# Kernel tuning notes

Hardware: AMD Instinct MI355X
Metric: run time of the kernel (lower is better)

## Reference

```python
import jax, jax.numpy as jnp
import numpy as np

NPOINT = 1024
BRANCHES = [(0.4, 32), (0.8, 64)]  # (radius, nsample)
SPECS = [[67, 64, 64, 128], [67, 64, 128, 256]]  # mlp specs after use_xyz (+3)
EPS = 1e-5


def setup_inputs() -> dict:
    key = jax.random.key(0)
    ks = jax.random.split(key, 16)
    B, N, C = 8, 8192, 64
    inp = {
        "xyz": jax.random.normal(ks[0], (B, N, 3), jnp.float32),
        "features": jax.random.normal(ks[1], (B, C, N), jnp.float32),
    }
    ki = 2
    for bi, spec in enumerate(SPECS):
        for li in range(3):
            o, i = spec[li + 1], spec[li]
            inp[f"w{bi}_{li}"] = jax.random.normal(ks[ki], (o, i), jnp.float32) * (1.0 / np.sqrt(i)); ki += 1
            inp[f"g{bi}_{li}"] = jnp.ones((o,), jnp.float32)
            inp[f"b{bi}_{li}"] = jnp.zeros((o,), jnp.float32)
    return inp


def fps(pts, npoint):
    # pts: [B, N+1, 3] (mean point prepended); sequential farthest point sampling
    B, N1, _ = pts.shape

    def step(carry, _):
        dist, far = carry
        idx3 = jnp.broadcast_to(far[:, None, None], (B, 1, 3))
        centroid = jnp.take_along_axis(pts, idx3, axis=1)  # [B,1,3]
        d = jnp.sum((pts - centroid) ** 2, axis=-1)        # [B,N+1]
        dist = jnp.minimum(dist, d)
        far2 = jnp.argmax(dist, axis=-1)
        return (dist, far2), centroid[:, 0, :]

    dist0 = jnp.full((B, N1), 1e10, jnp.float32)
    far0 = jnp.zeros((B,), jnp.int32)
    _, locs = jax.lax.scan(step, (dist0, far0), None, length=npoint)
    return jnp.transpose(locs, (1, 0, 2))  # [B, npoint, 3]


def ball_query(xyz, new_xyz, radius, nsample):
    # first <=nsample indices with dist^2 < radius^2, padded with first valid (0 if none)
    B, N, _ = xyz.shape
    d2 = jnp.sum((new_xyz[:, :, None, :] - xyz[:, None, :, :]) ** 2, axis=-1)  # [B,S,N]
    score = jnp.where(d2 < radius * radius, jnp.arange(N, dtype=jnp.int32), N)
    vals, _ = jax.lax.top_k(-score, nsample)  # smallest scores = earliest valid indices
    idx = -vals                               # [B,S,nsample], N marks invalid
    first = idx[..., :1]
    first = jnp.where(first < N, first, 0)
    return jnp.where(idx < N, idx, first)


def _forward(xyz, features, params):
    mean = jnp.mean(xyz, axis=1, keepdims=True)
    pts = jnp.concatenate([mean, xyz], axis=1)          # prepend mean point
    new_xyz = jax.lax.stop_gradient(fps(pts, NPOINT))   # [B,npoint,3] (torch no_grad)
    outs = []
    for (radius, nsample), layers in zip(BRANCHES, params):
        idx = ball_query(xyz, new_xyz, radius, nsample)           # [B,S,K]
        gxyz = jax.vmap(lambda p, i: p[i])(xyz, idx)              # [B,S,K,3]
        rel = jnp.transpose(gxyz - new_xyz[:, :, None, :], (0, 3, 1, 2))  # [B,3,S,K]
        gfeat = jax.vmap(lambda f, i: f[:, i])(features, idx)     # [B,C,S,K]
        x = jnp.concatenate([rel, gfeat], axis=1)                 # [B,3+C,S,K]
        for W, g, b in layers:  # Conv2d 1x1 (no bias) + BatchNorm (train stats) + ReLU
            x = jnp.einsum('oi,bisk->bosk', W, x)
            m = jnp.mean(x, axis=(0, 2, 3), keepdims=True)
            v = jnp.var(x, axis=(0, 2, 3), keepdims=True)
            x = (x - m) / jnp.sqrt(v + EPS) * g[None, :, None, None] + b[None, :, None, None]
            x = jax.nn.relu(x)
        outs.append(jnp.max(x, axis=3))                           # [B,Cout,S]
    return new_xyz, jnp.concatenate(outs, axis=1)


def reference(xyz, features,
              w0_0, g0_0, b0_0, w0_1, g0_1, b0_1, w0_2, g0_2, b0_2,
              w1_0, g1_0, b1_0, w1_1, g1_1, b1_1, w1_2, g1_2, b1_2):
    params = [
        [(w0_0, g0_0, b0_0), (w0_1, g0_1, b0_1), (w0_2, g0_2, b0_2)],
        [(w1_0, g1_0, b1_0), (w1_1, g1_1, b1_1), (w1_2, g1_2, b1_2)],
    ]
    return _forward(xyz, features, params)
```

## Files before the change

kernel.cpp:

```cpp
#include <hip/hip_runtime.h>
#include <hip/hip_bf16.h>
#include <cstdint>


typedef __attribute__((ext_vector_type(8))) short short8;
typedef __attribute__((ext_vector_type(4))) float f32x4;
typedef __attribute__((ext_vector_type(2))) float f32x2;

__device__ __forceinline__ float bf2f(unsigned short u) {
    return __uint_as_float(((unsigned)u) << 16);
}
__device__ __forceinline__ unsigned short f2bf(float f) {
    unsigned u = __float_as_uint(f);
    return (unsigned short)((u + 0x7fffu + ((u >> 16) & 1u)) >> 16);
}

__device__ __forceinline__ float wave_red_max_f32(float v) {
#define DPPSTEP(ctrl)                                                                  \
    {                                                                                  \
        int _t = __builtin_amdgcn_update_dpp((int)0xFF800000, __float_as_int(v), ctrl, \
                                             0xf, 0xf, false);                         \
        v = fmaxf(v, __int_as_float(_t));                                              \
    }
    DPPSTEP(0x111) DPPSTEP(0x112) DPPSTEP(0x114) DPPSTEP(0x118) DPPSTEP(0x142) DPPSTEP(0x143)
#undef DPPSTEP
    return v;
}
__device__ __forceinline__ unsigned wave_red_min_u32(unsigned v) {
#define DPPSTEP(ctrl)                                                                   \
    {                                                                                   \
        unsigned _t = (unsigned)__builtin_amdgcn_update_dpp((int)0xFFFFFFFF, (int)v,    \
                                                            ctrl, 0xf, 0xf, false);     \
        v = v < _t ? v : _t;                                                            \
    }
    DPPSTEP(0x111) DPPSTEP(0x112) DPPSTEP(0x114) DPPSTEP(0x118) DPPSTEP(0x142) DPPSTEP(0x143)
#undef DPPSTEP
    return v;
}
__device__ __forceinline__ unsigned long long u64max(unsigned long long a, unsigned long long b) {
    return a > b ? a : b;
}
__device__ __forceinline__ unsigned u32min(unsigned a, unsigned b) { return a < b ? a : b; }

static const size_t OFF_WBF   = 0;
static const size_t OFF_STATS = 262144;
static const size_t STATS_BYTES = 720896;
static const size_t OFF_AFF   = 1048576;
static const size_t OFF_IDX0  = 2097152;
static const size_t OFF_IDX1  = 3145728;
static const size_t OFF_MX    = 5242880;
static const size_t OFF_MN    = 13631488;
static const size_t OFF_Y0    = 22020096;
static const size_t OFF_Y1    = 90177536;
static const size_t OFF_FEATT = 211812352;

__global__ __launch_bounds__(512) void fused_pre(
    const float* __restrict__ xyz, const float* __restrict__ feat,
    float* __restrict__ newxyz, unsigned short* __restrict__ ft,
    const float* __restrict__ w0, const float* __restrict__ w1, const float* __restrict__ w2,
    const float* __restrict__ w3, const float* __restrict__ w4, const float* __restrict__ w5,
    unsigned short* __restrict__ wb) {
    __shared__ union alignas(16) SM {
        struct {
            float ptsx[8200], ptsy[8200], ptsz[8200];
            float ldsM[16][3];
            float meanv[3];
            unsigned long long sKey[2][8];
            float cbuf[3072];
        } f;
        float tile[64][65];
    } sm;
    const int tid = threadIdx.x;

    if (blockIdx.x >= 1032) {
        int id = (int)(blockIdx.x - 1032) * 512 + tid;
        const int psz[6] = {6144, 4096, 8192, 6144, 8192, 32768};
        const int Kp[6] = {96, 64, 64, 96, 64, 128};
        const int Ks[6] = {67, 64, 64, 67, 64, 128};
        const float* wp[6] = {w0, w1, w2, w3, w4, w5};
        int off = 0;
        for (int l = 0; l < 6; ++l) {
            if (id < off + psz[l]) {
                int e = id - off;
                int m = e / Kp[l], k = e - m * Kp[l];
                float v = (k < Ks[l]) ? wp[l][m * Ks[l] + k] : 0.f;
                wb[id] = f2bf(v);
                return;
            }
            off += psz[l];
        }
        return;
    }

    if (blockIdx.x >= 8) {
        int tb = (int)blockIdx.x - 8;
        int b = tb >> 7;
        int j0 = (tb & 127) * 64;
#pragma unroll
        for (int i = 0; i < 8; ++i) {
            int e = i * 512 + tid;
            int c = e >> 6, j = e & 63;
            sm.tile[j][c] = feat[((size_t)b * 64 + c) * 8192 + j0 + j];
        }
        __syncthreads();
#pragma unroll
        for (int i = 0; i < 8; ++i) {
            int e = i * 512 + tid;
            int j = e >> 6, c = e & 63;
            ft[((size_t)(b * 8192 + j0 + j)) * 96 + 3 + c] = f2bf(sm.tile[j][c]);
        }
        if (tid < 64) {
            int j = tid;
            size_t base = ((size_t)(b * 8192 + j0 + j)) * 96;
            const float* xp = xyz + ((size_t)b * 8192 + j0 + j) * 3;
            ft[base + 0] = f2bf(xp[0]);
            ft[base + 1] = f2bf(xp[1]);
            ft[base + 2] = f2bf(xp[2]);
        } else if (tid < 128) {
            int j = tid - 64;
            size_t base = ((size_t)(b * 8192 + j0 + j)) * 96;
            for (int c = 67; c < 96; ++c) ft[base + c] = 0;
        }
        return;
    }

    const int b = blockIdx.x;
    const int t = tid;
    const int lane = t & 63, wv = t >> 6;
    const float* xb = xyz + (size_t)b * 8192 * 3;

    f32x2 px[8], py[8], pz[8], d[8];
#pragma unroll
    for (int k = 0; k < 8; ++k) {
        int q0 = t + 512 * (2 * k);
        int q1 = t + 512 * (2 * k + 1);
        px[k].x = xb[q0 * 3 + 0]; px[k].y = xb[q1 * 3 + 0];
        py[k].x = xb[q0 * 3 + 1]; py[k].y = xb[q1 * 3 + 1];
        pz[k].x = xb[q0 * 3 + 2]; pz[k].y = xb[q1 * 3 + 2];
        d[k].x = 1e10f; d[k].y = 1e10f;
        sm.f.ptsx[q0 + 1] = px[k].x; sm.f.ptsx[q1 + 1] = px[k].y;
        sm.f.ptsy[q0 + 1] = py[k].x; sm.f.ptsy[q1 + 1] = py[k].y;
        sm.f.ptsz[q0 + 1] = pz[k].x; sm.f.ptsz[q1 + 1] = pz[k].y;
    }
    float sxA = 0.f, syA = 0.f, szA = 0.f;
    float sxB = 0.f, syB = 0.f, szB = 0.f;
    int uA = (t + 1023) & 1023;
    int uB = (t + 511) & 1023;
#pragma unroll
    for (int j = 0; j < 8; ++j) {
        int ia = uA + 1024 * j;
        int ib = uB + 1024 * j;
        sxA += xb[ia * 3 + 0]; syA += xb[ia * 3 + 1]; szA += xb[ia * 3 + 2];
        sxB += xb[ib * 3 + 0]; syB += xb[ib * 3 + 1]; szB += xb[ib * 3 + 2];
    }
#pragma unroll
    for (int off = 32; off; off >>= 1) {
        sxA += __shfl_xor(sxA, off, 64);
        syA += __shfl_xor(syA, off, 64);
        szA += __shfl_xor(szA, off, 64);
        sxB += __shfl_xor(sxB, off, 64);
        syB += __shfl_xor(syB, off, 64);
        szB += __shfl_xor(szB, off, 64);
    }
    if (lane == 0) {
        sm.f.ldsM[wv][0] = sxA; sm.f.ldsM[wv][1] = syA; sm.f.ldsM[wv][2] = szA;
        sm.f.ldsM[wv + 8][0] = sxB; sm.f.ldsM[wv + 8][1] = syB; sm.f.ldsM[wv + 8][2] = szB;
    }
    __syncthreads();
    if (t < 3) {
        float s = 0.f;
        for (int w = 0; w < 16; ++w) s += sm.f.ldsM[w][t];
        sm.f.meanv[t] = s * (1.f / 8192.f);
    }
    __syncthreads();
    float cx = sm.f.meanv[0], cy = sm.f.meanv[1], cz = sm.f.meanv[2];
    const float mmx = cx, mmy = cy, mmz = cz;
    float dm = 1e10f;
    if (t == 0) { sm.f.ptsx[0] = cx; sm.f.ptsy[0] = cy; sm.f.ptsz[0] = cz; }
    __syncthreads();

    for (int it = 0; it < 1024; ++it) {
        if (t == 0) {
            sm.f.cbuf[it * 3 + 0] = cx;
            sm.f.cbuf[it * 3 + 1] = cy;
            sm.f.cbuf[it * 3 + 2] = cz;
        }
        f32x2 c0, c1, c2, vm2;
        c0.x = cx; c0.y = cx; c1.x = cy; c1.y = cy; c2.x = cz; c2.y = cz;
        vm2.x = -1e30f; vm2.y = -1e30f;
        {
#pragma clang fp contract(off)
#pragma unroll
            for (int k = 0; k < 8; ++k) {
                f32x2 dx = px[k] - c0;
                f32x2 dy = py[k] - c1;
                f32x2 dz = pz[k] - c2;
                f32x2 dd = (dx * dx + dy * dy) + dz * dz;
                f32x2 nd = __builtin_elementwise_min(d[k], dd);
                d[k] = nd;
                vm2 = __builtin_elementwise_max(vm2, nd);
            }
        }
        float vmax = fmaxf(vm2.x, vm2.y);
        if (t == 0) {
            float dx = __fsub_rn(mmx, cx);
            float dy = __fsub_rn(mmy, cy);
            float dz = __fsub_rn(mmz, cz);
            float dd = __fadd_rn(__fadd_rn(__fmul_rn(dx, dx), __fmul_rn(dy, dy)), __fmul_rn(dz, dz));
            dm = fminf(dm, dd);
            vmax = fmaxf(vmax, dm);
        }
        float wm = wave_red_max_f32(vmax);
        float bmaxw = __int_as_float(__builtin_amdgcn_readlane(__float_as_int(wm), 63));
        unsigned m2[8];
#pragma unroll
        for (int k = 0; k < 8; ++k) {
            unsigned i0 = (d[k].x == bmaxw) ? (unsigned)(t + 512 * (2 * k) + 1) : 0xFFFFFFFFu;
            unsigned i1 = (d[k].y == bmaxw) ? (unsigned)(t + 512 * (2 * k + 1) + 1) : 0xFFFFFFFFu;
            m2[k] = u32min(i0, i1);
        }
        unsigned n0 = u32min(m2[0], m2[1]), n1 = u32min(m2[2], m2[3]);
        unsigned n2 = u32min(m2[4], m2[5]), n3 = u32min(m2[6], m2[7]);
        unsigned mi = u32min(u32min(n0, n1), u32min(n2, n3));
        if (t == 0 && dm == bmaxw) mi = 0u;
        unsigned wmin = wave_red_min_u32(mi);
        unsigned miw = (unsigned)__builtin_amdgcn_readlane((int)wmin, 63);
        int par = it & 1;
        if (lane == 0)
            sm.f.sKey[par][wv] = ((unsigned long long)__float_as_uint(bmaxw) << 32) |
                                 (unsigned long long)(8192u - miw);
        __syncthreads();
        unsigned long long ka[8];
#pragma unroll
        for (int i = 0; i < 8; ++i) ka[i] = sm.f.sKey[par][i];
        unsigned long long p0 = u64max(ka[0], ka[1]), p1 = u64max(ka[2], ka[3]);
        unsigned long long p2 = u64max(ka[4], ka[5]), p3 = u64max(ka[6], ka[7]);
        unsigned long long kk = u64max(u64max(p0, p1), u64max(p2, p3));
        int far = 8192 - (int)(unsigned)(kk & 0xffffffffull);
        cx = sm.f.ptsx[far];
        cy = sm.f.ptsy[far];
        cz = sm.f.ptsz[far];
    }
    __syncthreads();
    float* ob = newxyz + (size_t)b * 3072;
#pragma unroll
    for (int i = 0; i < 6; ++i) ob[t + 512 * i] = sm.f.cbuf[t + 512 * i];
}

__global__ void ball_query_kernel(const float* __restrict__ xyz, const float* __restrict__ newxyz,
                                  int* __restrict__ idxout, float r2, int K) {
    int wid = (blockIdx.x * blockDim.x + threadIdx.x) >> 6;
    int lane = threadIdx.x & 63;
    int b = wid >> 10;
    const float* q = newxyz + (size_t)wid * 3;
    float qx = q[0], qy = q[1], qz = q[2];
    const float* xb = xyz + (size_t)b * 8192 * 3;
    int* out = idxout + (size_t)wid * K;
    int count = 0;
    int first = 0;
    for (int base = 0; base < 8192 && count < K; base += 64) {
        int j = base + lane;
        float dx = __fsub_rn(xb[j * 3 + 0], qx);
        float dy = __fsub_rn(xb[j * 3 + 1], qy);
        float dz = __fsub_rn(xb[j * 3 + 2], qz);
        float d2 = __fadd_rn(__fadd_rn(__fmul_rn(dx, dx), __fmul_rn(dy, dy)), __fmul_rn(dz, dz));
        bool in = d2 < r2;
        unsigned long long m = __ballot(in);
        if (count == 0 && m) first = base + __ffsll((long long)m) - 1;
        if (in) {
            int pos = count + __popcll(m & ((1ull << lane) - 1ull));
            if (pos < K) out[pos] = j;
        }
        count += __popcll(m);
    }
    if (count < K) {
        int fillv = (count > 0) ? first : 0;
        for (int p = count + lane; p < K; p += 64) out[p] = fillv;
    }
}

template <int Mp, int Kp, int IN_MODE, int OUT_MODE, int KSH>
__global__ __launch_bounds__(256) void gemm_mfma(
    const unsigned short* __restrict__ Wb, const unsigned short* __restrict__ Xin,
    const float* __restrict__ aff, const int* __restrict__ idx,
    const unsigned short* __restrict__ ftp, const float* __restrict__ newxyz,
    unsigned short* __restrict__ Yout, float* __restrict__ MX, float* __restrict__ MN,
    float* __restrict__ statS, float* __restrict__ statQ) {
    constexpr int MT = Mp / 64;
    constexpr int KS = Kp / 32;
    constexpr int Kpad = Kp + 8;
    constexpr int KC = Kp / 8;
    constexpr int CPT = (64 * KC) / 256;
    __shared__ unsigned short Bs[64 * Kpad];
    __shared__ float sAux[256];
    int* sAuxI = (int*)sAux;

    const int tid = threadIdx.x;
    const int w = tid >> 6;
    const int lane = tid & 63;
    const int n = lane & 15;
    const int quad = lane >> 4;
    const int rbase = w * (Mp / 4);
    const long col0 = (long)blockIdx.x * 64;

    short8 a[MT][KS];
#pragma unroll
    for (int mt = 0; mt < MT; ++mt)
#pragma unroll
        for (int ks = 0; ks < KS; ++ks)
            a[mt][ks] = *(const short8*)(Wb + (size_t)(rbase + mt * 16 + n) * Kp + ks * 32 + quad * 8);

    if constexpr (IN_MODE == 0) {
        if (tid < 64) {
            long colg = col0 + tid;
            sAuxI[tid] = idx[colg];
            long sk = colg >> KSH;
            sAux[64 + tid] = newxyz[sk * 3 + 0];
            sAux[128 + tid] = newxyz[sk * 3 + 1];
            sAux[192 + tid] = newxyz[sk * 3 + 2];
        }
    } else {
        if (tid < 2 * Kp) sAux[tid] = aff[tid];
    }
    __syncthreads();

    if constexpr (IN_MODE == 0) {
        const int bb = (int)(col0 >> (KSH + 10));
#pragma unroll
        for (int i = 0; i < CPT; ++i) {
            int c = i * 256 + tid;
            int col = c / KC;
            int kc = c - col * KC;
            int j = sAuxI[col];
            short8 v = *(const short8*)(ftp + ((long)(bb * 8192 + j)) * 96 + kc * 8);
            if (kc == 0) {
                v[0] = (short)f2bf(bf2f((unsigned short)v[0]) - sAux[64 + col]);
                v[1] = (short)f2bf(bf2f((unsigned short)v[1]) - sAux[128 + col]);
                v[2] = (short)f2bf(bf2f((unsigned short)v[2]) - sAux[192 + col]);
            }
            *(short8*)(&Bs[col * Kpad + kc * 8]) = v;
        }
    } else {
#pragma unroll
        for (int i = 0; i < CPT; ++i) {
            int c = i * 256 + tid;
            int col = c / KC;
            int kc = c - col * KC;
            short8 raw = *(const short8*)(Xin + (col0 + col) * (long)Kp + kc * 8);
            short8 v;
#pragma unroll
            for (int e = 0; e < 8; ++e) {
                float xf = bf2f((unsigned short)raw[e]);
                xf = fmaxf(fmaf(xf, sAux[kc * 8 + e], sAux[Kp + kc * 8 + e]), 0.f);
                v[e] = (short)f2bf(xf);
            }
            *(short8*)(&Bs[col * Kpad + kc * 8]) = v;
        }
    }
    __syncthreads();

    f32x4 acc[MT][4];
#pragma unroll
    for (int mt = 0; mt < MT; ++mt)
#pragma unroll
        for (int nt = 0; nt < 4; ++nt)
#pragma unroll
            for (int r = 0; r < 4; ++r) acc[mt][nt][r] = 0.f;

#pragma unroll
    for (int ks = 0; ks < KS; ++ks) {
#pragma unroll
        for (int nt = 0; nt < 4; ++nt) {
            short8 bfr = *(const short8*)(&Bs[(nt * 16 + n) * Kpad + ks * 32 + quad * 8]);
#pragma unroll
            for (int mt = 0; mt < MT; ++mt)
                acc[mt][nt] = __builtin_amdgcn_mfma_f32_16x16x32_bf16(a[mt][ks], bfr, acc[mt][nt], 0, 0, 0);
        }
    }

    const int slot = (int)(blockIdx.x & 127);
#pragma unroll
    for (int mt = 0; mt < MT; ++mt)
#pragma unroll
        for (int r = 0; r < 4; ++r) {
            float s = 0.f, q = 0.f;
#pragma unroll
            for (int nt = 0; nt < 4; ++nt) {
                float v = acc[mt][nt][r];
                s += v;
                q = fmaf(v, v, q);
            }
#pragma unroll
            for (int off = 1; off < 16; off <<= 1) {
                s += __shfl_xor(s, off, 16);
                q += __shfl_xor(q, off, 16);
            }
            if (n == 0) {
                int ch = rbase + mt * 16 + quad * 4 + r;
                atomicAdd(statS + (size_t)ch * 128 + slot, s);
                atomicAdd(statQ + (size_t)ch * 128 + slot, q);
            }
        }

    if constexpr (OUT_MODE == 0) {
#pragma unroll
        for (int mt = 0; mt < MT; ++mt)
#pragma unroll
            for (int nt = 0; nt < 4; ++nt) {
                long col = col0 + nt * 16 + n;
                unsigned p0 = f2bf(acc[mt][nt][0]) | ((unsigned)f2bf(acc[mt][nt][1]) << 16);
                unsigned p1 = f2bf(acc[mt][nt][2]) | ((unsigned)f2bf(acc[mt][nt][3]) << 16);
                uint2 st; st.x = p0; st.y = p1;
                *(uint2*)(Yout + col * Mp + rbase + mt * 16 + quad * 4) = st;
            }
    } else {
#pragma unroll
        for (int mt = 0; mt < MT; ++mt)
#pragma unroll
            for (int r = 0; r < 4; ++r) {
                if constexpr (KSH == 6) {
                    float mx = acc[mt][0][r], mn = acc[mt][0][r];
#pragma unroll
                    for (int nt = 1; nt < 4; ++nt) {
                        mx = fmaxf(mx, acc[mt][nt][r]);
                        mn = fminf(mn, acc[mt][nt][r]);
                    }
#pragma unroll
                    for (int off = 1; off < 16; off <<= 1) {
                        mx = fmaxf(mx, __shfl_xor(mx, off, 16));
                        mn = fminf(mn, __shfl_xor(mn, off, 16));
                    }
                    if (n == 0) {
                        int ch = rbase + mt * 16 + quad * 4 + r;
                        long g = col0 >> 6;
                        MX[(long)ch * 8192 + g] = mx;
                        MN[(long)ch * 8192 + g] = mn;
                    }
                } else {
#pragma unroll
                    for (int gh = 0; gh < 2; ++gh) {
                        float mx = fmaxf(acc[mt][2 * gh][r], acc[mt][2 * gh + 1][r]);
                        float mn = fminf(acc[mt][2 * gh][r], acc[mt][2 * gh + 1][r]);
#pragma unroll
                        for (int off = 1; off < 16; off <<= 1) {
                            mx = fmaxf(mx, __shfl_xor(mx, off, 16));
                            mn = fminf(mn, __shfl_xor(mn, off, 16));
                        }
                        if (n == 0) {
                            int ch = rbase + mt * 16 + quad * 4 + r;
                            long g = (col0 >> 5) + gh;
                            MX[(long)ch * 8192 + g] = mx;
                            MN[(long)ch * 8192 + g] = mn;
                        }
                    }
                }
            }
    }
}

__global__ void finalize_kernel(const float* __restrict__ sS, const float* __restrict__ sQ,
                                const float* __restrict__ g, const float* __restrict__ b,
                                float* __restrict__ aff, int C, float invCount) {
    int c = threadIdx.x + blockIdx.x * blockDim.x;
    if (c >= C) return;
    float s = 0.f, q = 0.f;
    for (int k = 0; k < 128; ++k) { s += sS[c * 128 + k]; q += sQ[c * 128 + k]; }
    float mean = s * invCount;
    float var = fmaxf(q * invCount - mean * mean, 0.f);
    float sc = g[c] / sqrtf(var + 1e-5f);
    float sh = b[c] - mean * sc;
    aff[c] = sc;
    aff[C + c] = sh;
}

__global__ void final_out_kernel(const float* __restrict__ MX, const float* __restrict__ MN,
                                 const float* __restrict__ aff, float* __restrict__ out1,
                                 int Cout, int cOff) {
    long i = (long)blockIdx.x * 256 + threadIdx.x;
    int c = (int)(i >> 13);
    int gidx = (int)(i & 8191);
    int b = gidx >> 10, s = gidx & 1023;
    float sc = aff[c], sh = aff[Cout + c];
    float v = fmaxf(fmaxf(sc * MX[i] + sh, sc * MN[i] + sh), 0.f);
    out1[((long)b * 384 + cOff + c) * 1024 + s] = v;
}

extern "C" void kernel_launch(void* const* d_in, const int* in_sizes, int n_in,
                              void* d_out, int out_size, void* d_ws, size_t ws_size,
                              hipStream_t stream) {
    const float* xyz = (const float*)d_in[0];
    const float* feat = (const float*)d_in[1];
    const float *W[6], *G[6], *Bi[6];
    for (int l = 0; l < 6; ++l) {
        W[l] = (const float*)d_in[2 + l * 3];
        G[l] = (const float*)d_in[3 + l * 3];
        Bi[l] = (const float*)d_in[4 + l * 3];
    }
    char* ws = (char*)d_ws;
    float* out0 = (float*)d_out;
    float* out1 = (float*)d_out + 24576;

    unsigned short* wb = (unsigned short*)(ws + OFF_WBF);
    float* stats = (float*)(ws + OFF_STATS);
    float* affine = (float*)(ws + OFF_AFF);
    int* idx0 = (int*)(ws + OFF_IDX0);
    int* idx1 = (int*)(ws + OFF_IDX1);
    float* mx = (float*)(ws + OFF_MX);
    float* mn = (float*)(ws + OFF_MN);
    unsigned short* y0 = (unsigned short*)(ws + OFF_Y0);
    unsigned short* y1 = (unsigned short*)(ws + OFF_Y1);
    unsigned short* ftp = (unsigned short*)(ws + OFF_FEATT);

    hipMemsetAsync(stats, 0, STATS_BYTES, stream);
    fused_pre<<<1160, 512, 0, stream>>>(xyz, feat, out0, ftp, W[0], W[1], W[2], W[3], W[4],
                                        W[5], wb);

    const int wOff[6] = {0, 6144, 10240, 18432, 24576, 32768};
    int stOff[6], afOff[6];
    {
        const int Cs[6] = {64, 64, 128, 64, 128, 256};
        int so = 0, ao = 0;
        for (int l = 0; l < 6; ++l) {
            stOff[l] = so; so += Cs[l] * 256;
            afOff[l] = ao; ao += Cs[l] * 2;
        }
    }

    for (int br = 0; br < 2; ++br) {
        const int K = br ? 64 : 32;
        const float radius = br ? 0.8f : 0.4f;
        const long NCOL = 8L * 1024 * K;
        int* idx = br ? idx1 : idx0;
        const int l0 = br * 3, l1 = br * 3 + 1, l2 = br * 3 + 2;
        const int M2 = br ? 256 : 128;
        const float invCount = 1.f / (float)NCOL;
        const int nblk = (int)(NCOL / 64);

        ball_query_kernel<<<2048, 256, 0, stream>>>(xyz, out0, idx, radius * radius, K);

        if (br == 0) {
            gemm_mfma<64, 96, 0, 0, 5><<<nblk, 256, 0, stream>>>(
                wb + wOff[l0], nullptr, nullptr, idx, ftp, out0, y0, nullptr, nullptr,
                stats + stOff[l0], stats + stOff[l0] + 64 * 128);
            finalize_kernel<<<1, 256, 0, stream>>>(stats + stOff[l0], stats + stOff[l0] + 64 * 128,
                                                   G[l0], Bi[l0], affine + afOff[l0], 64, invCount);
            gemm_mfma<64, 64, 1, 0, 5><<<nblk, 256, 0, stream>>>(
                wb + wOff[l1], y0, affine + afOff[l0], nullptr, nullptr, nullptr, y1, nullptr,
                nullptr, stats + stOff[l1], stats + stOff[l1] + 64 * 128);
            finalize_kernel<<<1, 256, 0, stream>>>(stats + stOff[l1], stats + stOff[l1] + 64 * 128,
                                                   G[l1], Bi[l1], affine + afOff[l1], 64, invCount);
            gemm_mfma<128, 64, 1, 1, 5><<<nblk, 256, 0, stream>>>(
                wb + wOff[l2], y1, affine + afOff[l1], nullptr, nullptr, nullptr, nullptr, mx, mn,
                stats + stOff[l2], stats + stOff[l2] + 128 * 128);
            finalize_kernel<<<1, 256, 0, stream>>>(stats + stOff[l2], stats + stOff[l2] + 128 * 128,
                                                   G[l2], Bi[l2], affine + afOff[l2], 128, invCount);
        } else {
            gemm_mfma<64, 96, 0, 0, 6><<<nblk, 256, 0, stream>>>(
                wb + wOff[l0], nullptr, nullptr, idx, ftp, out0, y0, nullptr, nullptr,
                stats + stOff[l0], stats + stOff[l0] + 64 * 128);
            finalize_kernel<<<1, 256, 0, stream>>>(stats + stOff[l0], stats + stOff[l0] + 64 * 128,
                                                   G[l0], Bi[l0], affine + afOff[l0], 64, invCount);
            gemm_mfma<128, 64, 1, 0, 6><<<nblk, 256, 0, stream>>>(
                wb + wOff[l1], y0, affine + afOff[l0], nullptr, nullptr, nullptr, y1, nullptr,
                nullptr, stats + stOff[l1], stats + stOff[l1] + 128 * 128);
            finalize_kernel<<<1, 256, 0, stream>>>(stats + stOff[l1], stats + stOff[l1] + 128 * 128,
                                                   G[l1], Bi[l1], affine + afOff[l1], 128, invCount);
            gemm_mfma<256, 128, 1, 1, 6><<<nblk, 256, 0, stream>>>(
                wb + wOff[l2], y1, affine + afOff[l1], nullptr, nullptr, nullptr, nullptr, mx, mn,
                stats + stOff[l2], stats + stOff[l2] + 256 * 128);
            finalize_kernel<<<1, 256, 0, stream>>>(stats + stOff[l2], stats + stOff[l2] + 256 * 128,
                                                   G[l2], Bi[l2], affine + afOff[l2], 256, invCount);
        }

        final_out_kernel<<<(M2 * 8192) / 256, 256, 0, stream>>>(mx, mn, affine + afOff[l2], out1,
                                                                M2, br ? 128 : 0);
    }
}
```

Baseline: 1.783 ms.

## Merge ball queries into one launch and store B tiles in MFMA fragment order

The two per-branch ball-query launches become a single kernel with 4096 blocks, where the block index selects radius, K and output buffer. This removes one launch and lets both branches' queries run concurrently. The GEMM's shared-memory B tile now uses an MFMA-fragment-ordered layout, so each lane reads a contiguous short8 at (nt*KS+ks)*64+lane, replacing the padded row-major layout. This aims to cut LDS bank conflicts and address arithmetic on the MFMA read side, at the cost of more scattered global gathers during staging.

After: 1.765 ms. No clear change (-1.0%).

```diff
diff --git a/kernel.cpp b/kernel.cpp
--- a/kernel.cpp
+++ b/kernel.cpp
@@ -247,9 +247,14 @@
     for (int i = 0; i < 6; ++i) ob[t + 512 * i] = sm.f.cbuf[t + 512 * i];
 }
 
-__global__ void ball_query_kernel(const float* __restrict__ xyz, const float* __restrict__ newxyz,
-                                  int* __restrict__ idxout, float r2, int K) {
-    int wid = (blockIdx.x * blockDim.x + threadIdx.x) >> 6;
+__global__ void ball_query2(const float* __restrict__ xyz, const float* __restrict__ newxyz,
+                            int* __restrict__ idx0, int* __restrict__ idx1) {
+    int bid = blockIdx.x;
+    int br = (bid >= 2048);
+    int K = br ? 64 : 32;
+    float r2 = br ? (0.8f * 0.8f) : (0.4f * 0.4f);
+    int* idxout = br ? idx1 : idx0;
+    int wid = (((bid & 2047) * 256) + threadIdx.x) >> 6;
     int lane = threadIdx.x & 63;
     int b = wid >> 10;
     const float* q = newxyz + (size_t)wid * 3;
@@ -288,10 +293,7 @@
     float* __restrict__ statS, float* __restrict__ statQ) {
     constexpr int MT = Mp / 64;
     constexpr int KS = Kp / 32;
-    constexpr int Kpad = Kp + 8;
-    constexpr int KC = Kp / 8;
-    constexpr int CPT = (64 * KC) / 256;
-    __shared__ unsigned short Bs[64 * Kpad];
+    __shared__ unsigned short Bs[256 * KS * 8];
     __shared__ float sAux[256];
     int* sAuxI = (int*)sAux;
 
@@ -324,38 +326,37 @@
     }
     __syncthreads();
 
-    if constexpr (IN_MODE == 0) {
-        const int bb = (int)(col0 >> (KSH + 10));
-#pragma unroll
-        for (int i = 0; i < CPT; ++i) {
-            int c = i * 256 + tid;
-            int col = c / KC;
-            int kc = c - col * KC;
+#pragma unroll
+    for (int i = 0; i < KS; ++i) {
+        int p = i * 256 + tid;
+        int pl = p & 63;
+        int pn = pl & 15;
+        int pq = pl >> 4;
+        int rest = p >> 6;
+        int pks = rest % KS;
+        int pnt = rest / KS;
+        int col = pnt * 16 + pn;
+        int kc = pks * 4 + pq;
+        short8 v;
+        if constexpr (IN_MODE == 0) {
+            const int bb = (int)(col0 >> (KSH + 10));
             int j = sAuxI[col];
-            short8 v = *(const short8*)(ftp + ((long)(bb * 8192 + j)) * 96 + kc * 8);
+            v = *(const short8*)(ftp + ((long)(bb * 8192 + j)) * 96 + kc * 8);
             if (kc == 0) {
                 v[0] = (short)f2bf(bf2f((unsigned short)v[0]) - sAux[64 + col]);
                 v[1] = (short)f2bf(bf2f((unsigned short)v[1]) - sAux[128 + col]);
                 v[2] = (short)f2bf(bf2f((unsigned short)v[2]) - sAux[192 + col]);
             }
-            *(short8*)(&Bs[col * Kpad + kc * 8]) = v;
-        }
-    } else {
-#pragma unroll
-        for (int i = 0; i < CPT; ++i) {
-            int c = i * 256 + tid;
-            int col = c / KC;
-            int kc = c - col * KC;
+        } else {
             short8 raw = *(const short8*)(Xin + (col0 + col) * (long)Kp + kc * 8);
-            short8 v;
 #pragma unroll
             for (int e = 0; e < 8; ++e) {
                 float xf = bf2f((unsigned short)raw[e]);
                 xf = fmaxf(fmaf(xf, sAux[kc * 8 + e], sAux[Kp + kc * 8 + e]), 0.f);
                 v[e] = (short)f2bf(xf);
             }
-            *(short8*)(&Bs[col * Kpad + kc * 8]) = v;
-        }
+        }
+        *(short8*)(&Bs[p * 8]) = v;
     }
     __syncthreads();
 
@@ -371,7 +372,7 @@
     for (int ks = 0; ks < KS; ++ks) {
 #pragma unroll
         for (int nt = 0; nt < 4; ++nt) {
-            short8 bfr = *(const short8*)(&Bs[(nt * 16 + n) * Kpad + ks * 32 + quad * 8]);
+            short8 bfr = *(const short8*)(&Bs[((nt * KS + ks) * 64 + lane) * 8]);
 #pragma unroll
             for (int mt = 0; mt < MT; ++mt)
                 acc[mt][nt] = __builtin_amdgcn_mfma_f32_16x16x32_bf16(a[mt][ks], bfr, acc[mt][nt], 0, 0, 0);
@@ -514,6 +515,7 @@
     hipMemsetAsync(stats, 0, STATS_BYTES, stream);
     fused_pre<<<1160, 512, 0, stream>>>(xyz, feat, out0, ftp, W[0], W[1], W[2], W[3], W[4],
                                         W[5], wb);
+    ball_query2<<<4096, 256, 0, stream>>>(xyz, out0, idx0, idx1);
 
     const int wOff[6] = {0, 6144, 10240, 18432, 24576, 32768};
     int stOff[6], afOff[6];
@@ -528,15 +530,12 @@
 
     for (int br = 0; br < 2; ++br) {
         const int K = br ? 64 : 32;
-        const float radius = br ? 0.8f : 0.4f;
         const long NCOL = 8L * 1024 * K;
         int* idx = br ? idx1 : idx0;
         const int l0 = br * 3, l1 = br * 3 + 1, l2 = br * 3 + 2;
         const int M2 = br ? 256 : 128;
         const float invCount = 1.f / (float)NCOL;
         const int nblk = (int)(NCOL / 64);
-
-        ball_query_kernel<<<2048, 256, 0, stream>>>(xyz, out0, idx, radius * radius, K);
 
         if (br == 0) {
             gemm_mfma<64, 96, 0, 0, 5><<<nblk, 256, 0, stream>>>(
```
